# Performance work log

Measured on AMD Instinct MI355X. Metric: run time of the kernel, lower is better.

The kernel has to match this reference:

```python
import jax, jax.numpy as jnp
import numpy as np

HEADS = 4
DIM_HEAD = 32
SCALE = 16.0
EPS = 1e-5  # jax.nn.standardize default


def _standardize(t):
    # standardize over last axis (the flattened x*y*z sequence), per (b, h, d)
    mu = jnp.mean(t, axis=-1, keepdims=True)
    var = jnp.var(t, axis=-1, keepdims=True)
    return (t - mu) * jax.lax.rsqrt(var + EPS)


def setup_inputs() -> dict:
    key = jax.random.key(0)
    k1, k2, k3 = jax.random.split(key, 3)
    dim = 64
    hidden = HEADS * DIM_HEAD  # 128
    b, x, y, z = 2, 16, 16, 16
    inp = jax.random.normal(k1, (b, x, y, z, dim), dtype=jnp.float32)
    # 1x1x1 convs == pointwise channel matmuls; init like flax lecun_normal-ish scale
    w_qkv = jax.random.normal(k2, (dim, 3 * hidden), dtype=jnp.float32) / np.sqrt(dim)
    w_out = jax.random.normal(k3, (hidden, dim), dtype=jnp.float32) / np.sqrt(hidden)
    b_out = jnp.zeros((dim,), dtype=jnp.float32)
    return {"input": inp, "w_qkv": w_qkv, "w_out": w_out, "b_out": b_out}


def reference(input, w_qkv, w_out, b_out):
    b, x, y, z, c = input.shape
    s = x * y * z
    # pointwise conv -> qkv
    qkv = jnp.einsum('bxyzc,cd->bxyzd', input, w_qkv)  # [b,x,y,z,3*hidden]
    q, k, v = jnp.split(qkv, 3, axis=-1)
    # rearrange 'b x y z (h c) -> b h c (x y z)'
    def to_bhds(t):
        return t.reshape(b, s, HEADS, DIM_HEAD).transpose(0, 2, 3, 1)  # [b,h,d,s]
    q, k, v = map(to_bhds, (q, k, v))
    q = _standardize(q)
    k = _standardize(k)
    sim = jnp.einsum('bhdi,bhdj->bhij', q, k) * SCALE  # [b,h,s,s]
    attn = jax.nn.softmax(sim, axis=-1)
    out = jnp.einsum('bhij,bhdj->bhid', attn, v)  # [b,h,s,d]
    # rearrange 'b h (x y z) d -> b x y z (h d)'
    out = out.transpose(0, 2, 1, 3).reshape(b, x, y, z, HEADS * DIM_HEAD)
    return jnp.einsum('bxyzc,co->bxyzo', out, w_out) + b_out
```

## Files before the change

kernel.cpp:

```cpp
#include <hip/hip_runtime.h>
#include <math.h>
#include <stdint.h>


typedef __attribute__((ext_vector_type(8))) short short8;
typedef __attribute__((ext_vector_type(2))) float f32x2;
typedef __attribute__((ext_vector_type(4))) float f32x4;
typedef __attribute__((ext_vector_type(16))) float f32x16;

#define QSCALE 23.083120654223414f

#if __has_builtin(__builtin_amdgcn_exp2f)
#define EXP2F(x) __builtin_amdgcn_exp2f(x)
#else
#define EXP2F(x) exp2f(x)
#endif

__device__ inline uint32_t pack_hilo(float y) {
  uint32_t uy = __float_as_uint(y);
  uint32_t hb = (uy + 0x7fffu + ((uy >> 16) & 1u)) >> 16;
  float hf = __uint_as_float(hb << 16);
  float r = y - hf;
  uint32_t ur = __float_as_uint(r);
  uint32_t lb = (ur + 0x7fffu + ((ur >> 16) & 1u)) >> 16;
  return (hb << 16) | (lb & 0xffffu);
}

__device__ inline ushort f32_to_bf16(float y) {
  uint32_t uy = __float_as_uint(y);
  return (ushort)((uy + 0x7fffu + ((uy >> 16) & 1u)) >> 16);
}

__device__ inline float bpermf(int addr, float v) {
  return __int_as_float(__builtin_amdgcn_ds_bpermute(addr, __float_as_int(v)));
}

__device__ inline short8 as_s8(uint4 v) {
  union { uint4 u; short8 s; } t;
  t.u = v;
  return t.s;
}

__global__ __launch_bounds__(256) void qkv_kernel(const float* __restrict__ in,
                                                  const float* __restrict__ w,
                                                  float* __restrict__ qf,
                                                  float* __restrict__ kf,
                                                  ushort* __restrict__ vfr,
                                                  float* __restrict__ psum,
                                                  float* __restrict__ psq,
                                                  const float* __restrict__ bias,
                                                  float* __restrict__ out) {
  __shared__ char smem[18432];
  __shared__ float ssum[64], ssq[64];
  ushort* Bh = (ushort*)smem;
  ushort* Bl = (ushort*)(smem + 9216);
  float* VT = (float*)smem;

  const int ctile = blockIdx.x % 6;
  const int stile = blockIdx.x / 6;
  const int tid = threadIdx.x;
  const int row0 = stile * 64;
  const int sel = ctile >> 1;

  for (int i = blockIdx.x * 256 + tid; i < 8192 * 64; i += 768 * 256)
    out[i] = bias[i & 63];

  if (tid < 64) { ssum[tid] = 0.f; ssq[tid] = 0.f; }

  {
    const int col = tid & 63;
    const int k0 = (tid >> 6) * 16;
    const float* wp = w + (size_t)k0 * 384 + ctile * 64 + col;
    float xv[16];
#pragma unroll
    for (int j = 0; j < 16; ++j) xv[j] = wp[(size_t)j * 384];
    uint32_t hi[8], lo[8];
#pragma unroll
    for (int p = 0; p < 8; ++p) {
      const uint32_t u0 = __float_as_uint(xv[2 * p]);
      const uint32_t u1 = __float_as_uint(xv[2 * p + 1]);
      hi[p] = __builtin_amdgcn_perm(u1, u0, 0x07060302u);
      const float d0 = xv[2 * p] - __uint_as_float(u0 & 0xffff0000u);
      const float d1 = xv[2 * p + 1] - __uint_as_float(u1 & 0xffff0000u);
      lo[p] = __builtin_amdgcn_perm(__float_as_uint(d1), __float_as_uint(d0), 0x07060302u);
    }
    uint4* bh = (uint4*)&Bh[col * 72 + k0];
    bh[0] = make_uint4(hi[0], hi[1], hi[2], hi[3]);
    bh[1] = make_uint4(hi[4], hi[5], hi[6], hi[7]);
    uint4* bl = (uint4*)&Bl[col * 72 + k0];
    bl[0] = make_uint4(lo[0], lo[1], lo[2], lo[3]);
    bl[1] = make_uint4(lo[4], lo[5], lo[6], lo[7]);
  }
  __syncthreads();

  const int wv = tid >> 6, lane = tid & 63;
  const int wr = wv >> 1, wc = wv & 1;
  const int h2 = lane >> 5, pl = lane & 31;

  short8 ah[4], al[4];
  {
    const float* ap = in + (size_t)(row0 + wr * 32 + pl) * 64 + h2 * 8;
#pragma unroll
    for (int kb = 0; kb < 4; ++kb) {
      const float4 xa = *(const float4*)(ap + kb * 16);
      const float4 xb = *(const float4*)(ap + kb * 16 + 4);
      const float xs[8] = {xa.x, xa.y, xa.z, xa.w, xb.x, xb.y, xb.z, xb.w};
      uint32_t hp[4], lp[4];
#pragma unroll
      for (int p = 0; p < 4; ++p) {
        const uint32_t u0 = __float_as_uint(xs[2 * p]);
        const uint32_t u1 = __float_as_uint(xs[2 * p + 1]);
        hp[p] = __builtin_amdgcn_perm(u1, u0, 0x07060302u);
        const float d0 = xs[2 * p] - __uint_as_float(u0 & 0xffff0000u);
        const float d1 = xs[2 * p + 1] - __uint_as_float(u1 & 0xffff0000u);
        lp[p] = __builtin_amdgcn_perm(__float_as_uint(d1), __float_as_uint(d0), 0x07060302u);
      }
      union { uint32_t u[4]; short8 s; } th, tl;
      th.u[0] = hp[0]; th.u[1] = hp[1]; th.u[2] = hp[2]; th.u[3] = hp[3];
      tl.u[0] = lp[0]; tl.u[1] = lp[1]; tl.u[2] = lp[2]; tl.u[3] = lp[3];
      ah[kb] = th.s;
      al[kb] = tl.s;
    }
  }

  const ushort* bhp = &Bh[(wc * 32 + pl) * 72 + h2 * 8];
  const ushort* blp = &Bl[(wc * 32 + pl) * 72 + h2 * 8];
  f32x16 acc = {};
#pragma unroll
  for (int kb = 0; kb < 4; ++kb) {
    const short8 bh = *(const short8*)(bhp + kb * 16);
    const short8 bl = *(const short8*)(blp + kb * 16);
    acc = __builtin_amdgcn_mfma_f32_32x32x16_bf16(ah[kb], bh, acc, 0, 0, 0);
    acc = __builtin_amdgcn_mfma_f32_32x32x16_bf16(ah[kb], bl, acc, 0, 0, 0);
    acc = __builtin_amdgcn_mfma_f32_32x32x16_bf16(al[kb], bh, acc, 0, 0, 0);
  }

  const int b = row0 >> 12;
  const int sl0 = (row0 & 4095) + wr * 32;
  const int chg = ctile * 64 + wc * 32 + pl;

  if (sel < 2) {
    const int hd0 = chg & 127;
    const int h = hd0 >> 5, d0 = hd0 & 31;
    float* dst = (sel == 0 ? qf : kf) + ((size_t)(b * 4 + h) * 4096 + sl0) * 32 + d0;
    float s1 = 0.f, s2 = 0.f;
#pragma unroll
    for (int reg = 0; reg < 16; ++reg) {
      const int r = (reg & 3) + 8 * (reg >> 2) + 4 * h2;
      dst[(size_t)r * 32] = acc[reg];
      s1 += acc[reg];
      s2 += acc[reg] * acc[reg];
    }
    atomicAdd(&ssum[wc * 32 + pl], s1);
    atomicAdd(&ssq[wc * 32 + pl], s2);
    __syncthreads();
    if (tid < 64) {
      const int ch = (ctile & 1) * 64 + tid;
      const int idx = (((sel * 2 + b) * 128) + ch) * 64 + (stile & 63);
      psum[idx] = ssum[tid];
      psq[idx] = ssq[tid];
    }
  } else {
    __syncthreads();
    const int chv = wc * 32 + pl;
#pragma unroll
    for (int reg = 0; reg < 16; ++reg) {
      const int r = wr * 32 + (reg & 3) + 8 * (reg >> 2) + 4 * h2;
      VT[chv * 68 + r] = acc[reg];
    }
    __syncthreads();
    const int jt0 = (row0 & 4095) >> 5;
#pragma unroll
    for (int hl = 0; hl < 2; ++hl) {
      const int jtl = tid >> 7, c = (tid >> 6) & 1, ln = tid & 63;
      const int d = ln & 31, hh = ln >> 5;
      const int jloc = 32 * jtl + 16 * c + 8 * hh;
      const int ch = hl * 32 + d;
      const float4 f0 = *(const float4*)&VT[ch * 68 + jloc];
      const float4 f1 = *(const float4*)&VT[ch * 68 + jloc + 4];
      uint4 pk;
      pk.x = (uint32_t)f32_to_bf16(f0.x) | ((uint32_t)f32_to_bf16(f0.y) << 16);
      pk.y = (uint32_t)f32_to_bf16(f0.z) | ((uint32_t)f32_to_bf16(f0.w) << 16);
      pk.z = (uint32_t)f32_to_bf16(f1.x) | ((uint32_t)f32_to_bf16(f1.y) << 16);
      pk.w = (uint32_t)f32_to_bf16(f1.z) | ((uint32_t)f32_to_bf16(f1.w) << 16);
      const int h = (ctile - 4) * 2 + hl;
      ushort* dst =
          vfr + (((size_t)((b * 4 + h) * 128 + jt0 + jtl) * 2 + c) * 64 + ln) * 8;
      *(uint4*)dst = pk;
    }
  }
}

__global__ __launch_bounds__(256) void norm_kernel(const float* __restrict__ kf,
                                                   ushort* __restrict__ kfr_hi,
                                                   ushort* __restrict__ kfr_lo,
                                                   const float* __restrict__ psum,
                                                   const float* __restrict__ psq) {
  const int bx = blockIdx.x;
  const int bh = bx >> 4;
  const int s0 = (bx & 15) * 256;
  const int tid = threadIdx.x;
  __shared__ float red[2][32][8];
  __shared__ float tA[32], tB[32];
  {
    const int d = tid >> 3, p = tid & 7;
    const int base = ((2 + (bh >> 2)) * 128 + (bh & 3) * 32 + d) * 64 + p * 8;
    float sm = 0.f, sq = 0.f;
#pragma unroll
    for (int e = 0; e < 8; ++e) {
      sm += psum[base + e];
      sq += psq[base + e];
    }
    red[0][d][p] = sm;
    red[1][d][p] = sq;
  }
  __syncthreads();
  if (tid < 32) {
    float sm = 0.f, sq = 0.f;
#pragma unroll
    for (int e = 0; e < 8; ++e) {
      sm += red[0][tid][e];
      sq += red[1][tid][e];
    }
    const float mu = sm * (1.f / 4096.f);
    const float inv = rsqrtf(sq * (1.f / 4096.f) - mu * mu + 1e-5f);
    tA[tid] = inv;
    tB[tid] = -mu * inv;
  }
  __syncthreads();

  const float* src = kf + (size_t)bh * 4096 * 32;
  ushort* dhi = kfr_hi + (size_t)(bh * 128 + (s0 >> 5)) * 1024;
  ushort* dlo = kfr_lo + (size_t)(bh * 128 + (s0 >> 5)) * 1024;
#pragma unroll
  for (int pass = 0; pass < 4; ++pass) {
    const int idx = tid + pass * 256;
    const int jtl = idx >> 7;
    const int c = (idx >> 6) & 1;
    const int ln = idx & 63;
    const int p = ln & 31, hh = ln >> 5;
    const int row = (p & 0x13) | ((p & 4) << 1) | ((p & 8) >> 1);
    const int s = s0 + 32 * jtl + row;
    const int d0 = 16 * c + 8 * hh;
    const float4 x0 = *(const float4*)&src[(size_t)s * 32 + d0];
    const float4 x1 = *(const float4*)&src[(size_t)s * 32 + d0 + 4];
    const float4 A0 = *(const float4*)&tA[d0];
    const float4 A1 = *(const float4*)&tA[d0 + 4];
    const float4 B0 = *(const float4*)&tB[d0];
    const float4 B1 = *(const float4*)&tB[d0 + 4];
    uint32_t pk[8];
    pk[0] = pack_hilo(fmaf(x0.x, A0.x, B0.x));
    pk[1] = pack_hilo(fmaf(x0.y, A0.y, B0.y));
    pk[2] = pack_hilo(fmaf(x0.z, A0.z, B0.z));
    pk[3] = pack_hilo(fmaf(x0.w, A0.w, B0.w));
    pk[4] = pack_hilo(fmaf(x1.x, A1.x, B1.x));
    pk[5] = pack_hilo(fmaf(x1.y, A1.y, B1.y));
    pk[6] = pack_hilo(fmaf(x1.z, A1.z, B1.z));
    pk[7] = pack_hilo(fmaf(x1.w, A1.w, B1.w));
    uint4 HV, LV;
    HV.x = __builtin_amdgcn_perm(pk[1], pk[0], 0x07060302u);
    HV.y = __builtin_amdgcn_perm(pk[3], pk[2], 0x07060302u);
    HV.z = __builtin_amdgcn_perm(pk[5], pk[4], 0x07060302u);
    HV.w = __builtin_amdgcn_perm(pk[7], pk[6], 0x07060302u);
    LV.x = __builtin_amdgcn_perm(pk[1], pk[0], 0x05040100u);
    LV.y = __builtin_amdgcn_perm(pk[3], pk[2], 0x05040100u);
    LV.z = __builtin_amdgcn_perm(pk[5], pk[4], 0x05040100u);
    LV.w = __builtin_amdgcn_perm(pk[7], pk[6], 0x05040100u);
    const size_t doff = ((size_t)(jtl * 2 + c) * 64 + ln) * 8;
    *(uint4*)(dhi + doff) = HV;
    *(uint4*)(dlo + doff) = LV;
  }
}

__global__ __launch_bounds__(256, 2) void attn_kernel(const float* __restrict__ qf,
                                                      const float* __restrict__ psum,
                                                      const float* __restrict__ psq,
                                                      const ushort* __restrict__ kfr_hi,
                                                      const ushort* __restrict__ kfr_lo,
                                                      const ushort* __restrict__ vfr,
                                                      const float* __restrict__ wout,
                                                      float* __restrict__ out) {
  __shared__ float OM[4 * 2 * 32 * 36];
  __shared__ float ML[4 * 2 * 64];
  __shared__ float tAB[64];

  const int tid = threadIdx.x;
  const int w = tid >> 6;
  const int lane = tid & 63;
  const int pl = lane & 31, h2 = lane >> 5;
  const int bh = blockIdx.x & 7;
  const int itp = blockIdx.x >> 3;

  {
    const int d = tid >> 3, p = tid & 7;
    const int base = ((bh >> 2) * 128 + (bh & 3) * 32 + d) * 64 + p * 8;
    float sm = 0.f, sq = 0.f;
#pragma unroll
    for (int e = 0; e < 8; ++e) {
      sm += psum[base + e];
      sq += psq[base + e];
    }
    ML[d * 8 + p] = sm;
    ML[256 + d * 8 + p] = sq;
  }
  __syncthreads();
  if (tid < 32) {
    float sm = 0.f, sq = 0.f;
#pragma unroll
    for (int e = 0; e < 8; ++e) {
      sm += ML[tid * 8 + e];
      sq += ML[256 + tid * 8 + e];
    }
    const float mu = sm * (1.f / 4096.f);
    const float inv = rsqrtf(sq * (1.f / 4096.f) - mu * mu + 1e-5f) * QSCALE;
    tAB[tid] = inv;
    tAB[32 + tid] = -mu * inv;
  }
  __syncthreads();

  short8 qfrag_h[2][2], qfrag_l[2][2];
  {
    const float* qsrc = qf + (size_t)bh * 4096 * 32;
#pragma unroll
    for (int itl = 0; itl < 2; ++itl) {
      const int s = (itp * 2 + itl) * 32 + pl;
#pragma unroll
      for (int c = 0; c < 2; ++c) {
        const int d0 = 16 * c + 8 * h2;
        const float4 x0 = *(const float4*)&qsrc[(size_t)s * 32 + d0];
        const float4 x1 = *(const float4*)&qsrc[(size_t)s * 32 + d0 + 4];
        const float4 A0 = *(const float4*)&tAB[d0];
        const float4 A1 = *(const float4*)&tAB[d0 + 4];
        const float4 B0 = *(const float4*)&tAB[32 + d0];
        const float4 B1 = *(const float4*)&tAB[32 + d0 + 4];
        uint32_t pk[8];
        pk[0] = pack_hilo(fmaf(x0.x, A0.x, B0.x));
        pk[1] = pack_hilo(fmaf(x0.y, A0.y, B0.y));
        pk[2] = pack_hilo(fmaf(x0.z, A0.z, B0.z));
        pk[3] = pack_hilo(fmaf(x0.w, A0.w, B0.w));
        pk[4] = pack_hilo(fmaf(x1.x, A1.x, B1.x));
        pk[5] = pack_hilo(fmaf(x1.y, A1.y, B1.y));
        pk[6] = pack_hilo(fmaf(x1.z, A1.z, B1.z));
        pk[7] = pack_hilo(fmaf(x1.w, A1.w, B1.w));
        union { uint32_t u[4]; short8 s8; } hv, lv;
        hv.u[0] = __builtin_amdgcn_perm(pk[1], pk[0], 0x07060302u);
        hv.u[1] = __builtin_amdgcn_perm(pk[3], pk[2], 0x07060302u);
        hv.u[2] = __builtin_amdgcn_perm(pk[5], pk[4], 0x07060302u);
        hv.u[3] = __builtin_amdgcn_perm(pk[7], pk[6], 0x07060302u);
        lv.u[0] = __builtin_amdgcn_perm(pk[1], pk[0], 0x05040100u);
        lv.u[1] = __builtin_amdgcn_perm(pk[3], pk[2], 0x05040100u);
        lv.u[2] = __builtin_amdgcn_perm(pk[5], pk[4], 0x05040100u);
        lv.u[3] = __builtin_amdgcn_perm(pk[7], pk[6], 0x05040100u);
        qfrag_h[itl][c] = hv.s8;
        qfrag_l[itl][c] = lv.s8;
      }
    }
  }
  __syncthreads();

  const short8 qh0_0 = qfrag_h[0][0], qh1_0 = qfrag_h[0][1];
  const short8 ql0_0 = qfrag_l[0][0], ql1_0 = qfrag_l[0][1];
  const short8 qh0_1 = qfrag_h[1][0], qh1_1 = qfrag_h[1][1];
  const short8 ql0_1 = qfrag_l[1][0], ql1_1 = qfrag_l[1][1];

  const int bp32 = (lane ^ 32) << 2;

  const size_t kbase = (size_t)(bh * 128 + w * 32) * 1024 + lane * 8;
  const ushort* kh = kfr_hi + kbase;
  const ushort* kl = kfr_lo + kbase;
  const ushort* vp = vfr + kbase;

  union { f32x16 v; f32x2 p[8]; } oac0, oac1;
#pragma unroll
  for (int r = 0; r < 16; ++r) { oac0.v[r] = 0.f; oac1.v[r] = 0.f; }
  const f32x16 zf = {};
  float m0 = -INFINITY, l0 = 0.f, m1 = -INFINITY, l1 = 0.f;

  uint4 rk0 = *(const uint4*)(kh);
  uint4 rk1 = *(const uint4*)(kh + 512);
  uint4 rl0 = *(const uint4*)(kl);
  uint4 rl1 = *(const uint4*)(kl + 512);

  for (int t = 0; t < 32; ++t) {
    const short8 ck0 = as_s8(rk0), ck1 = as_s8(rk1);
    const short8 cl0 = as_s8(rl0), cl1 = as_s8(rl1);
    const uint4 rv0 = *(const uint4*)(vp + t * 1024);
    const uint4 rv1 = *(const uint4*)(vp + t * 1024 + 512);
    {
      const int off = (t + 1) * 1024;
      rk0 = *(const uint4*)(kh + off);
      rk1 = *(const uint4*)(kh + off + 512);
      rl0 = *(const uint4*)(kl + off);
      rl1 = *(const uint4*)(kl + off + 512);
    }
    const short8 cv0 = as_s8(rv0), cv1 = as_s8(rv1);

#pragma unroll
    for (int itl = 0; itl < 2; ++itl) {
      const short8 qh0 = itl == 0 ? qh0_0 : qh0_1;
      const short8 qh1 = itl == 0 ? qh1_0 : qh1_1;
      const short8 ql0 = itl == 0 ? ql0_0 : ql0_1;
      const short8 ql1 = itl == 0 ? ql1_0 : ql1_1;
      float m = itl == 0 ? m0 : m1;
      float l = itl == 0 ? l0 : l1;

      __builtin_amdgcn_s_setprio(1);
      union { f32x16 v; f32x2 p[8]; } sc;
      sc.v = __builtin_amdgcn_mfma_f32_32x32x16_bf16(ck0, qh0, zf, 0, 0, 0);
      sc.v = __builtin_amdgcn_mfma_f32_32x32x16_bf16(ck1, qh1, sc.v, 0, 0, 0);
      sc.v = __builtin_amdgcn_mfma_f32_32x32x16_bf16(ck0, ql0, sc.v, 0, 0, 0);
      sc.v = __builtin_amdgcn_mfma_f32_32x32x16_bf16(ck1, ql1, sc.v, 0, 0, 0);
      sc.v = __builtin_amdgcn_mfma_f32_32x32x16_bf16(cl0, qh0, sc.v, 0, 0, 0);
      sc.v = __builtin_amdgcn_mfma_f32_32x32x16_bf16(cl1, qh1, sc.v, 0, 0, 0);
      __builtin_amdgcn_s_setprio(0);

      const float x0 = fmaxf(fmaxf(sc.v[0], sc.v[1]), sc.v[2]);
      const float x1 = fmaxf(fmaxf(sc.v[3], sc.v[4]), sc.v[5]);
      const float x2 = fmaxf(fmaxf(sc.v[6], sc.v[7]), sc.v[8]);
      const float x3 = fmaxf(fmaxf(sc.v[9], sc.v[10]), sc.v[11]);
      const float x4 = fmaxf(fmaxf(sc.v[12], sc.v[13]), sc.v[14]);
      float mx = fmaxf(fmaxf(fmaxf(x0, x1), x2), fmaxf(fmaxf(x3, x4), sc.v[15]));
      mx = fmaxf(mx, bpermf(bp32, mx));
      const float mn = fmaxf(m, mx);
      const float al = EXP2F(m - mn);
      m = mn;
      const f32x2 mn2 = {mn, mn};
#pragma unroll
      for (int i = 0; i < 8; ++i) sc.p[i] = sc.p[i] - mn2;
#pragma unroll
      for (int r = 0; r < 16; ++r) sc.v[r] = EXP2F(sc.v[r]);
      const f32x2 a0 = sc.p[0] + sc.p[1], a1 = sc.p[2] + sc.p[3];
      const f32x2 a2 = sc.p[4] + sc.p[5], a3 = sc.p[6] + sc.p[7];
      const f32x2 b0 = a0 + a1, b1 = a2 + a3;
      const f32x2 c0 = b0 + b1;
      float rs = c0.x + c0.y;
      rs += bpermf(bp32, rs);
      l = l * al + rs;
      const f32x2 al2 = {al, al};

      uint32_t pk[8];
#pragma unroll
      for (int i = 0; i < 8; ++i)
        pk[i] = __builtin_amdgcn_perm(__float_as_uint(sc.v[2 * i + 1]),
                                      __float_as_uint(sc.v[2 * i]), 0x07060302u);
      union { uint32_t u4[4]; short8 s8; } p0, p1;
      p0.u4[0] = pk[0]; p0.u4[1] = pk[1]; p0.u4[2] = pk[2]; p0.u4[3] = pk[3];
      p1.u4[0] = pk[4]; p1.u4[1] = pk[5]; p1.u4[2] = pk[6]; p1.u4[3] = pk[7];

      if (itl == 0) {
#pragma unroll
        for (int i = 0; i < 8; ++i) oac0.p[i] = oac0.p[i] * al2;
        __builtin_amdgcn_s_setprio(1);
        oac0.v = __builtin_amdgcn_mfma_f32_32x32x16_bf16(cv0, p0.s8, oac0.v, 0, 0, 0);
        oac0.v = __builtin_amdgcn_mfma_f32_32x32x16_bf16(cv1, p1.s8, oac0.v, 0, 0, 0);
        __builtin_amdgcn_s_setprio(0);
        m0 = m; l0 = l;
      } else {
#pragma unroll
        for (int i = 0; i < 8; ++i) oac1.p[i] = oac1.p[i] * al2;
        __builtin_amdgcn_s_setprio(1);
        oac1.v = __builtin_amdgcn_mfma_f32_32x32x16_bf16(cv0, p0.s8, oac1.v, 0, 0, 0);
        oac1.v = __builtin_amdgcn_mfma_f32_32x32x16_bf16(cv1, p1.s8, oac1.v, 0, 0, 0);
        __builtin_amdgcn_s_setprio(0);
        m1 = m; l1 = l;
      }
    }
  }

#pragma unroll
  for (int itl = 0; itl < 2; ++itl) {
    float* om = OM + (size_t)((w * 2 + itl) * 32 + pl) * 36;
    const f32x16& oa = itl == 0 ? oac0.v : oac1.v;
#pragma unroll
    for (int g = 0; g < 4; ++g)
      *(float4*)&om[4 * h2 + 8 * g] =
          make_float4(oa[4 * g], oa[4 * g + 1], oa[4 * g + 2], oa[4 * g + 3]);
    if (h2 == 0) {
      ML[(w * 2 + itl) * 64 + pl] = itl == 0 ? m0 : m1;
      ML[(w * 2 + itl) * 64 + 32 + pl] = itl == 0 ? l0 : l1;
    }
  }
  __syncthreads();
  const int b = bh >> 2, h = bh & 3;
  float vals[8];
#pragma unroll
  for (int pass = 0; pass < 8; ++pass) {
    const int idx = tid + pass * 256;
    const int itl = idx >> 10;
    const int i = (idx >> 5) & 31;
    const int d = idx & 31;
    float mk[4], lk[4];
#pragma unroll
    for (int k = 0; k < 4; ++k) {
      mk[k] = ML[(k * 2 + itl) * 64 + i];
      lk[k] = ML[(k * 2 + itl) * 64 + 32 + i];
    }
    const float M = fmaxf(fmaxf(mk[0], mk[1]), fmaxf(mk[2], mk[3]));
    float L = 0.f, V = 0.f;
#pragma unroll
    for (int k = 0; k < 4; ++k) {
      const float wk = EXP2F(mk[k] - M);
      L += lk[k] * wk;
      V += OM[((k * 2 + itl) * 32 + i) * 36 + d] * wk;
    }
    vals[pass] = V * (1.001953125f / L);
  }
  __syncthreads();

  float* V2 = OM;
  float* WL = OM + 2048;
#pragma unroll
  for (int pass = 0; pass < 8; ++pass) V2[tid + pass * 256] = vals[pass];
  {
    const float* wsrc = wout + (size_t)h * 32 * 64;
#pragma unroll
    for (int p = 0; p < 8; ++p) WL[tid + p * 256] = wsrc[tid + p * 256];
  }
  __syncthreads();
#pragma unroll
  for (int p = 0; p < 16; ++p) {
    const int idx = tid + p * 256;
    const int itl = idx >> 11;
    const int i = (idx >> 6) & 31;
    const int col = idx & 63;
    float acc = 0.f;
#pragma unroll
    for (int d = 0; d < 32; ++d)
      acc = fmaf(V2[itl * 1024 + i * 32 + d], WL[d * 64 + col], acc);
    const int ig = (itp * 2 + itl) * 32 + i;
    atomicAdd(&out[((size_t)(b * 4096) + ig) * 64 + col], acc);
  }
}

extern "C" void kernel_launch(void* const* d_in, const int* in_sizes, int n_in,
                              void* d_out, int out_size, void* d_ws, size_t ws_size,
                              hipStream_t stream) {
  const float* input = (const float*)d_in[0];
  const float* w_qkv = (const float*)d_in[1];
  const float* w_out = (const float*)d_in[2];
  const float* b_out = (const float*)d_in[3];

  char* W = (char*)d_ws;
  float* qf = (float*)(W + 0);
  float* kf = (float*)(W + (4u << 20));
  ushort* kfr_hi = (ushort*)(W + (8u << 20));
  ushort* kfr_lo = (ushort*)(W + (10u << 20));
  ushort* vfr = (ushort*)(W + (12u << 20));
  float* psum = (float*)(W + (18u << 20));
  float* psq = (float*)(W + (18u << 20) + (128u << 10));
  float* out = (float*)d_out;

  hipLaunchKernelGGL(qkv_kernel, dim3(768), dim3(256), 0, stream, input, w_qkv, qf, kf,
                     vfr, psum, psq, b_out, out);
  hipLaunchKernelGGL(norm_kernel, dim3(128), dim3(256), 0, stream, kf, kfr_hi, kfr_lo,
                     psum, psq);
  hipLaunchKernelGGL(attn_kernel, dim3(512), dim3(256), 0, stream, qf, psum, psq,
                     kfr_hi, kfr_lo, vfr, w_out, out);
}
```

Before: 123.5 us.

## Fold key standardization into query scaling and drop the norm kernel

Keys are written raw as hi/lo bf16 fragments straight from the QKV projection kernel. The key mean is dropped because it only adds a per-row constant that softmax cancels, and the per-channel key inverse std is folded into the query scale inside the attention kernel. This removes the separate normalization launch and the fp32 key round trip through global memory. In exchange, raw (unstandardized) keys are split into bf16 hi/lo, which could change rounding behaviour slightly, and an extra barrier is added in the attention kernel.

```diff
diff --git a/kernel.cpp b/kernel.cpp
--- a/kernel.cpp
+++ b/kernel.cpp
@@ -44,7 +44,8 @@
 __global__ __launch_bounds__(256) void qkv_kernel(const float* __restrict__ in,
                                                   const float* __restrict__ w,
                                                   float* __restrict__ qf,
-                                                  float* __restrict__ kf,
+                                                  ushort* __restrict__ kfr_hi,
+                                                  ushort* __restrict__ kfr_lo,
                                                   ushort* __restrict__ vfr,
                                                   float* __restrict__ psum,
                                                   float* __restrict__ psq,
@@ -138,11 +139,12 @@
   const int b = row0 >> 12;
   const int sl0 = (row0 & 4095) + wr * 32;
   const int chg = ctile * 64 + wc * 32 + pl;
-
-  if (sel < 2) {
+  const int jt0 = (row0 & 4095) >> 5;
+
+  if (sel == 0) {
     const int hd0 = chg & 127;
     const int h = hd0 >> 5, d0 = hd0 & 31;
-    float* dst = (sel == 0 ? qf : kf) + ((size_t)(b * 4 + h) * 4096 + sl0) * 32 + d0;
+    float* dst = qf + ((size_t)(b * 4 + h) * 4096 + sl0) * 32 + d0;
     float s1 = 0.f, s2 = 0.f;
 #pragma unroll
     for (int reg = 0; reg < 16; ++reg) {
@@ -156,9 +158,57 @@
     __syncthreads();
     if (tid < 64) {
       const int ch = (ctile & 1) * 64 + tid;
-      const int idx = (((sel * 2 + b) * 128) + ch) * 64 + (stile & 63);
+      const int idx = ((b * 128) + ch) * 64 + (stile & 63);
       psum[idx] = ssum[tid];
       psq[idx] = ssq[tid];
+    }
+  } else if (sel == 1) {
+    float s1 = 0.f, s2 = 0.f;
+#pragma unroll
+    for (int reg = 0; reg < 16; ++reg) {
+      s1 += acc[reg];
+      s2 += acc[reg] * acc[reg];
+    }
+    atomicAdd(&ssum[wc * 32 + pl], s1);
+    atomicAdd(&ssq[wc * 32 + pl], s2);
+    __syncthreads();
+    const int chv = wc * 32 + pl;
+#pragma unroll
+    for (int reg = 0; reg < 16; ++reg) {
+      const int r = wr * 32 + (reg & 3) + 8 * (reg >> 2) + 4 * h2;
+      VT[chv * 68 + r] = acc[reg];
+    }
+    __syncthreads();
+    if (tid < 64) {
+      const int ch = (ctile & 1) * 64 + tid;
+      const int idx = (((2 + b) * 128) + ch) * 64 + (stile & 63);
+      psum[idx] = ssum[tid];
+      psq[idx] = ssq[tid];
+    }
+#pragma unroll
+    for (int hl = 0; hl < 2; ++hl) {
+      const int jtl = tid >> 7, c = (tid >> 6) & 1, ln = tid & 63;
+      const int p = ln & 31, hh = ln >> 5;
+      const int srow = 32 * jtl + ((p & 0x13) | ((p & 4) << 1) | ((p & 8) >> 1));
+      const int dbase = hl * 32 + 16 * c + 8 * hh;
+      uint32_t pk[8];
+#pragma unroll
+      for (int jj = 0; jj < 8; ++jj)
+        pk[jj] = pack_hilo(VT[(dbase + jj) * 68 + srow]);
+      uint4 HV, LV;
+      HV.x = __builtin_amdgcn_perm(pk[1], pk[0], 0x07060302u);
+      HV.y = __builtin_amdgcn_perm(pk[3], pk[2], 0x07060302u);
+      HV.z = __builtin_amdgcn_perm(pk[5], pk[4], 0x07060302u);
+      HV.w = __builtin_amdgcn_perm(pk[7], pk[6], 0x07060302u);
+      LV.x = __builtin_amdgcn_perm(pk[1], pk[0], 0x05040100u);
+      LV.y = __builtin_amdgcn_perm(pk[3], pk[2], 0x05040100u);
+      LV.z = __builtin_amdgcn_perm(pk[5], pk[4], 0x05040100u);
+      LV.w = __builtin_amdgcn_perm(pk[7], pk[6], 0x05040100u);
+      const int h = (ctile - 2) * 2 + hl;
+      const size_t doff =
+          (((size_t)((b * 4 + h) * 128 + jt0 + jtl) * 2 + c) * 64 + ln) * 8;
+      *(uint4*)(kfr_hi + doff) = HV;
+      *(uint4*)(kfr_lo + doff) = LV;
     }
   } else {
     __syncthreads();
@@ -169,7 +219,6 @@
       VT[chv * 68 + r] = acc[reg];
     }
     __syncthreads();
-    const int jt0 = (row0 & 4095) >> 5;
 #pragma unroll
     for (int hl = 0; hl < 2; ++hl) {
       const int jtl = tid >> 7, c = (tid >> 6) & 1, ln = tid & 63;
@@ -191,87 +240,6 @@
   }
 }
 
-__global__ __launch_bounds__(256) void norm_kernel(const float* __restrict__ kf,
-                                                   ushort* __restrict__ kfr_hi,
-                                                   ushort* __restrict__ kfr_lo,
-                                                   const float* __restrict__ psum,
-                                                   const float* __restrict__ psq) {
-  const int bx = blockIdx.x;
-  const int bh = bx >> 4;
-  const int s0 = (bx & 15) * 256;
-  const int tid = threadIdx.x;
-  __shared__ float red[2][32][8];
-  __shared__ float tA[32], tB[32];
-  {
-    const int d = tid >> 3, p = tid & 7;
-    const int base = ((2 + (bh >> 2)) * 128 + (bh & 3) * 32 + d) * 64 + p * 8;
-    float sm = 0.f, sq = 0.f;
-#pragma unroll
-    for (int e = 0; e < 8; ++e) {
-      sm += psum[base + e];
-      sq += psq[base + e];
-    }
-    red[0][d][p] = sm;
-    red[1][d][p] = sq;
-  }
-  __syncthreads();
-  if (tid < 32) {
-    float sm = 0.f, sq = 0.f;
-#pragma unroll
-    for (int e = 0; e < 8; ++e) {
-      sm += red[0][tid][e];
-      sq += red[1][tid][e];
-    }
-    const float mu = sm * (1.f / 4096.f);
-    const float inv = rsqrtf(sq * (1.f / 4096.f) - mu * mu + 1e-5f);
-    tA[tid] = inv;
-    tB[tid] = -mu * inv;
-  }
-  __syncthreads();
-
-  const float* src = kf + (size_t)bh * 4096 * 32;
-  ushort* dhi = kfr_hi + (size_t)(bh * 128 + (s0 >> 5)) * 1024;
-  ushort* dlo = kfr_lo + (size_t)(bh * 128 + (s0 >> 5)) * 1024;
-#pragma unroll
-  for (int pass = 0; pass < 4; ++pass) {
-    const int idx = tid + pass * 256;
-    const int jtl = idx >> 7;
-    const int c = (idx >> 6) & 1;
-    const int ln = idx & 63;
-    const int p = ln & 31, hh = ln >> 5;
-    const int row = (p & 0x13) | ((p & 4) << 1) | ((p & 8) >> 1);
-    const int s = s0 + 32 * jtl + row;
-    const int d0 = 16 * c + 8 * hh;
-    const float4 x0 = *(const float4*)&src[(size_t)s * 32 + d0];
-    const float4 x1 = *(const float4*)&src[(size_t)s * 32 + d0 + 4];
-    const float4 A0 = *(const float4*)&tA[d0];
-    const float4 A1 = *(const float4*)&tA[d0 + 4];
-    const float4 B0 = *(const float4*)&tB[d0];
-    const float4 B1 = *(const float4*)&tB[d0 + 4];
-    uint32_t pk[8];
-    pk[0] = pack_hilo(fmaf(x0.x, A0.x, B0.x));
-    pk[1] = pack_hilo(fmaf(x0.y, A0.y, B0.y));
-    pk[2] = pack_hilo(fmaf(x0.z, A0.z, B0.z));
-    pk[3] = pack_hilo(fmaf(x0.w, A0.w, B0.w));
-    pk[4] = pack_hilo(fmaf(x1.x, A1.x, B1.x));
-    pk[5] = pack_hilo(fmaf(x1.y, A1.y, B1.y));
-    pk[6] = pack_hilo(fmaf(x1.z, A1.z, B1.z));
-    pk[7] = pack_hilo(fmaf(x1.w, A1.w, B1.w));
-    uint4 HV, LV;
-    HV.x = __builtin_amdgcn_perm(pk[1], pk[0], 0x07060302u);
-    HV.y = __builtin_amdgcn_perm(pk[3], pk[2], 0x07060302u);
-    HV.z = __builtin_amdgcn_perm(pk[5], pk[4], 0x07060302u);
-    HV.w = __builtin_amdgcn_perm(pk[7], pk[6], 0x07060302u);
-    LV.x = __builtin_amdgcn_perm(pk[1], pk[0], 0x05040100u);
-    LV.y = __builtin_amdgcn_perm(pk[3], pk[2], 0x05040100u);
-    LV.z = __builtin_amdgcn_perm(pk[5], pk[4], 0x05040100u);
-    LV.w = __builtin_amdgcn_perm(pk[7], pk[6], 0x05040100u);
-    const size_t doff = ((size_t)(jtl * 2 + c) * 64 + ln) * 8;
-    *(uint4*)(dhi + doff) = HV;
-    *(uint4*)(dlo + doff) = LV;
-  }
-}
-
 __global__ __launch_bounds__(256, 2) void attn_kernel(const float* __restrict__ qf,
                                                       const float* __restrict__ psum,
                                                       const float* __restrict__ psq,
@@ -293,28 +261,38 @@
 
   {
     const int d = tid >> 3, p = tid & 7;
-    const int base = ((bh >> 2) * 128 + (bh & 3) * 32 + d) * 64 + p * 8;
-    float sm = 0.f, sq = 0.f;
+    const int bq = ((bh >> 2) * 128 + (bh & 3) * 32 + d) * 64 + p * 8;
+    const int bk = ((2 + (bh >> 2)) * 128 + (bh & 3) * 32 + d) * 64 + p * 8;
+    float qs = 0.f, qq = 0.f, ks = 0.f, kq = 0.f;
 #pragma unroll
     for (int e = 0; e < 8; ++e) {
-      sm += psum[base + e];
-      sq += psq[base + e];
-    }
-    ML[d * 8 + p] = sm;
-    ML[256 + d * 8 + p] = sq;
+      qs += psum[bq + e];
+      qq += psq[bq + e];
+      ks += psum[bk + e];
+      kq += psq[bk + e];
+    }
+    OM[tid] = qs;
+    OM[256 + tid] = qq;
+    OM[512 + tid] = ks;
+    OM[768 + tid] = kq;
   }
   __syncthreads();
   if (tid < 32) {
-    float sm = 0.f, sq = 0.f;
+    float qs = 0.f, qq = 0.f, ks = 0.f, kq = 0.f;
 #pragma unroll
     for (int e = 0; e < 8; ++e) {
-      sm += ML[tid * 8 + e];
-      sq += ML[256 + tid * 8 + e];
-    }
-    const float mu = sm * (1.f / 4096.f);
-    const float inv = rsqrtf(sq * (1.f / 4096.f) - mu * mu + 1e-5f) * QSCALE;
-    tAB[tid] = inv;
-    tAB[32 + tid] = -mu * inv;
+      qs += OM[tid * 8 + e];
+      qq += OM[256 + tid * 8 + e];
+      ks += OM[512 + tid * 8 + e];
+      kq += OM[768 + tid * 8 + e];
+    }
+    const float muQ = qs * (1.f / 4096.f);
+    const float invQ = rsqrtf(qq * (1.f / 4096.f) - muQ * muQ + 1e-5f);
+    const float muK = ks * (1.f / 4096.f);
+    const float invK = rsqrtf(kq * (1.f / 4096.f) - muK * muK + 1e-5f);
+    const float A = QSCALE * invQ * invK;
+    tAB[tid] = A;
+    tAB[32 + tid] = -muQ * A;
   }
   __syncthreads();
 
@@ -467,6 +445,7 @@
     }
   }
 
+  __syncthreads();
 #pragma unroll
   for (int itl = 0; itl < 2; ++itl) {
     float* om = OM + (size_t)((w * 2 + itl) * 32 + pl) * 36;
@@ -542,7 +521,6 @@
 
   char* W = (char*)d_ws;
   float* qf = (float*)(W + 0);
-  float* kf = (float*)(W + (4u << 20));
   ushort* kfr_hi = (ushort*)(W + (8u << 20));
   ushort* kfr_lo = (ushort*)(W + (10u << 20));
   ushort* vfr = (ushort*)(W + (12u << 20));
@@ -550,10 +528,8 @@
   float* psq = (float*)(W + (18u << 20) + (128u << 10));
   float* out = (float*)d_out;
 
-  hipLaunchKernelGGL(qkv_kernel, dim3(768), dim3(256), 0, stream, input, w_qkv, qf, kf,
-                     vfr, psum, psq, b_out, out);
-  hipLaunchKernelGGL(norm_kernel, dim3(128), dim3(256), 0, stream, kf, kfr_hi, kfr_lo,
-                     psum, psq);
+  hipLaunchKernelGGL(qkv_kernel, dim3(768), dim3(256), 0, stream, input, w_qkv, qf,
+                     kfr_hi, kfr_lo, vfr, psum, psq, b_out, out);
   hipLaunchKernelGGL(attn_kernel, dim3(512), dim3(256), 0, stream, qf, psum, psq,
                      kfr_hi, kfr_lo, vfr, w_out, out);
 }
```

Result: faster. 119.1 us (median of 2 runs) (-3.5%).
